# Kernel tuning notes

Measured on AMD Instinct MI355X. Metric: run time of the kernel, lower is better.

The kernel has to match this reference:

```python
import jax, jax.numpy as jnp
import numpy as np

B, T, G, P = 16, 256, 1024, 16          # batch, num_tf, num_genes, peaks per gene
N, GO_DIM = 4096, 6                      # num_gos, go_dim (hard-coded in module)
HEADS, OUT_CH = 2, 4                     # selfGATConv(go_dim, 4, heads=2)
E = 65536                                # num edges
NUM_OUT = 32


def lrelu(x, slope):
    return jnp.where(x >= 0, x, slope * x)


def setup_inputs() -> dict:
    ks = jax.random.split(jax.random.key(0), 12)
    x = jax.random.normal(ks[0], (B, T, G * P), dtype=jnp.float32)
    edge_index = jax.random.randint(ks[1], (2, E), 0, N, dtype=jnp.int64)
    # per-gene subNet: Linear(num_peak*num_tf, 1) -> weight [G, T, P], bias [G]
    W_sub = jax.random.normal(ks[2], (G, T, P), dtype=jnp.float32) * 0.02
    b_sub = jax.random.normal(ks[3], (G,), dtype=jnp.float32) * 0.02
    fc1_weight = jax.random.normal(ks[4], (N * GO_DIM, G), dtype=jnp.float32) * 0.02
    mask = (jax.random.uniform(ks[5], (N, G)) < 0.05).astype(jnp.float32)
    mask_rep = jnp.repeat(mask, GO_DIM, axis=0)  # [N*GO_DIM, G]
    fc1_bias = jax.random.normal(ks[6], (N * GO_DIM,), dtype=jnp.float32) * 0.02
    gat_weight = jax.random.normal(ks[7], (GO_DIM, HEADS * OUT_CH), dtype=jnp.float32) * 0.3
    gat_att = jax.random.normal(ks[8], (1, 1, HEADS, 2 * OUT_CH), dtype=jnp.float32) * 0.3
    gat_bias = jax.random.normal(ks[9], (OUT_CH,), dtype=jnp.float32) * 0.02
    out_weight = jax.random.normal(ks[10], (NUM_OUT, N * OUT_CH), dtype=jnp.float32) * 0.02
    out_bias = jax.random.normal(ks[11], (NUM_OUT,), dtype=jnp.float32) * 0.02
    return {"x": x, "edge_index": edge_index, "W_sub": W_sub, "b_sub": b_sub,
            "fc1_weight": fc1_weight, "mask_rep": mask_rep, "fc1_bias": fc1_bias,
            "gat_weight": gat_weight, "gat_att": gat_att, "gat_bias": gat_bias,
            "out_weight": out_weight, "out_bias": out_bias}


def reference(x, edge_index, W_sub, b_sub, fc1_weight, mask_rep, fc1_bias,
              gat_weight, gat_att, gat_bias, out_weight, out_bias):
    # --- per-gene subnets (uniform num_peaks -> block-diag as one einsum) ---
    xg = x.reshape(B, T, G, P)                        # contiguous cut blocks
    x_cat = jnp.einsum('btgp,gtp->bg', xg, W_sub) + b_sub   # [B, G]
    x_cat = lrelu(x_cat, 0.01)                        # nn.LeakyReLU default
    # --- masked dense linear -> GO-term hidden layer ---
    h = x_cat @ (fc1_weight * mask_rep).T + fc1_bias  # [B, N*GO_DIM]
    h = lrelu(h, 0.01)
    h = h.reshape(B, GO_DIM, N).transpose(2, 0, 1)    # [N, B, GO_DIM]
    # --- selfGATConv: gather -> leaky_relu score -> seg-softmax -> scatter-mean ---
    hn = (h @ gat_weight).reshape(N, B, HEADS, OUT_CH)  # [N, B, H, C]
    src, dst = edge_index[0], edge_index[1]
    x_j = hn[src]                                     # [E, B, H, C]
    x_i = hn[dst]
    att = gat_att[0, 0]                               # [H, 2C]
    alpha = (jnp.einsum('ebhc,hc->ebh', x_i, att[:, :OUT_CH]) +
             jnp.einsum('ebhc,hc->ebh', x_j, att[:, OUT_CH:]))
    alpha = lrelu(alpha, 0.2)                         # negative_slope=0.2
    amax = jax.ops.segment_max(alpha, dst, num_segments=N)
    alpha = jnp.exp(alpha - amax[dst])
    denom = jax.ops.segment_sum(alpha, dst, num_segments=N)
    alpha = alpha / denom[dst]                        # per-destination softmax
    msg = x_j * alpha[..., None]                      # [E, B, H, C]
    summed = jax.ops.segment_sum(msg, dst, num_segments=N)
    cnt = jax.ops.segment_sum(jnp.ones((E,), jnp.float32), dst, num_segments=N)
    aggr = summed / jnp.maximum(cnt, 1.0)[:, None, None, None]  # aggr='mean'
    aggr = aggr.mean(axis=2) + gat_bias               # concat=False: mean heads -> [N, B, C]
    # --- readout ---
    o = aggr.transpose(1, 2, 0).reshape(B, OUT_CH * N)
    o = lrelu(o, 0.01)                                # dropout is identity in eval
    return o @ out_weight.T + out_bias                # [B, NUM_OUT]
```

## Files before the change

### kernel.cpp

```cpp
#include <hip/hip_runtime.h>
#include <math.h>

#define KB 16
#define KT 256
#define KG 1024
#define KP 16
#define KN 4096
#define KGO 6
#define KH 2
#define KC 4
#define KE 65536
#define KOUT 32

__device__ __forceinline__ float lrelu(float x, float s) { return x >= 0.f ? x : s * x; }

__global__ __launch_bounds__(1024) void k1_subnet(const float* __restrict__ x,
                                                  const float* __restrict__ Wsub,
                                                  const float* __restrict__ bsub,
                                                  float* __restrict__ xcat,
                                                  int* __restrict__ cnt) {
    if (blockIdx.x >= 256) {
        int t = threadIdx.x;
#pragma unroll
        for (int i = 0; i < 4; ++i) cnt[t + i * 1024] = 0;
        return;
    }
    int wk  = ((blockIdx.x & 7) << 5) | (blockIdx.x >> 3);
    int tid = threadIdx.x;
    int sub = tid >> 8;
    int u   = tid & 255;
    int gc  = wk >> 4;
    int b   = wk & 15;
    int g0  = gc * 64;
    int g   = g0 + (u >> 2);
    int p4  = (u & 3) * 4;
    const float* xb = x + (size_t)b * (KT * KG * KP) + (size_t)g0 * KP + u * 4;
    const float* wg = Wsub + (size_t)g * (KT * KP) + p4;
    float4 acc = make_float4(0.f, 0.f, 0.f, 0.f);
    int t0 = sub * 64;
#pragma unroll 4
    for (int i = 0; i < 64; ++i) {
        int t = t0 + i;
        float4 xv = *(const float4*)(xb + (size_t)t * (KG * KP));
        float4 wv = *(const float4*)(wg + (size_t)t * KP);
        acc.x += xv.x * wv.x; acc.y += xv.y * wv.y;
        acc.z += xv.z * wv.z; acc.w += xv.w * wv.w;
    }
    float s = acc.x + acc.y + acc.z + acc.w;
    s += __shfl_xor(s, 1, 64);
    s += __shfl_xor(s, 2, 64);
    __shared__ float part[4][64];
    if ((u & 3) == 0) part[sub][u >> 2] = s;
    __syncthreads();
    if (tid < 64) {
        float v = part[0][tid] + part[1][tid] + part[2][tid] + part[3][tid];
        xcat[b * KG + g0 + tid] = lrelu(v + bsub[g0 + tid], 0.01f);
    }
}

__global__ __launch_bounds__(256) void k2_fc1(const float* __restrict__ w,
                                              const float* __restrict__ mask,
                                              const float* __restrict__ bias,
                                              const float* __restrict__ xcat,
                                              float* __restrict__ ht) {
    int wid = threadIdx.x >> 6;
    int lane = threadIdx.x & 63;
    int b0 = wid * 4;
    float4 xcr[4][4];
#pragma unroll
    for (int bb = 0; bb < 4; ++bb)
#pragma unroll
        for (int i = 0; i < 4; ++i)
            xcr[bb][i] = *(const float4*)(xcat + (b0 + bb) * KG + i * 256 + lane * 4);

    int mj_cur = -1;
    float4 mreg[4];
    for (int r = 0; r < 16; ++r) {
        int j = blockIdx.x * 16 + r;
        int mj = j / 6;
        if (mj != mj_cur) {
            const float* mr = mask + (size_t)(mj * 6) * KG;
#pragma unroll
            for (int i = 0; i < 4; ++i)
                mreg[i] = *(const float4*)(mr + i * 256 + lane * 4);
            mj_cur = mj;
        }
        const float* wr = w + (size_t)j * KG;
        float acc0 = 0.f, acc1 = 0.f, acc2 = 0.f, acc3 = 0.f;
#pragma unroll
        for (int i = 0; i < 4; ++i) {
            float4 wv = *(const float4*)(wr + i * 256 + lane * 4);
            float4 mv = mreg[i];
            float px = wv.x * mv.x, py = wv.y * mv.y, pz = wv.z * mv.z, pw = wv.w * mv.w;
            acc0 += px * xcr[0][i].x + py * xcr[0][i].y + pz * xcr[0][i].z + pw * xcr[0][i].w;
            acc1 += px * xcr[1][i].x + py * xcr[1][i].y + pz * xcr[1][i].z + pw * xcr[1][i].w;
            acc2 += px * xcr[2][i].x + py * xcr[2][i].y + pz * xcr[2][i].z + pw * xcr[2][i].w;
            acc3 += px * xcr[3][i].x + py * xcr[3][i].y + pz * xcr[3][i].z + pw * xcr[3][i].w;
        }
#pragma unroll
        for (int m = 1; m < 64; m <<= 1) {
            acc0 += __shfl_xor(acc0, m, 64);
            acc1 += __shfl_xor(acc1, m, 64);
            acc2 += __shfl_xor(acc2, m, 64);
            acc3 += __shfl_xor(acc3, m, 64);
        }
        if (lane == 0) {
            float bj = bias[j];
            int d = j >> 12;
            int n = j & 4095;
            float* hp = ht + ((size_t)n * KB) * KGO + d;
            hp[(b0 + 0) * KGO] = lrelu(acc0 + bj, 0.01f);
            hp[(b0 + 1) * KGO] = lrelu(acc1 + bj, 0.01f);
            hp[(b0 + 2) * KGO] = lrelu(acc2 + bj, 0.01f);
            hp[(b0 + 3) * KGO] = lrelu(acc3 + bj, 0.01f);
        }
    }
}

__global__ __launch_bounds__(256) void k3_gatw(const float* __restrict__ ht,
                                               const float* __restrict__ gw,
                                               const float* __restrict__ att,
                                               float* __restrict__ hn,
                                               float* __restrict__ si,
                                               float* __restrict__ sj) {
    __shared__ float cgw[48];
    __shared__ float catt[16];
    int t = threadIdx.x;
    if (t < 48) cgw[t] = gw[t];
    else if (t < 64) catt[t - 48] = att[t - 48];
    __syncthreads();
    int idx = blockIdx.x * 256 + t;
    float h6[6];
#pragma unroll
    for (int d = 0; d < 6; ++d) h6[d] = ht[(size_t)idx * KGO + d];
    float o[8];
#pragma unroll
    for (int hc = 0; hc < 8; ++hc) {
        float v = 0.f;
#pragma unroll
        for (int d = 0; d < 6; ++d) v += h6[d] * cgw[d * 8 + hc];
        o[hc] = v;
        hn[(size_t)idx * 8 + hc] = v;
    }
#pragma unroll
    for (int hh = 0; hh < 2; ++hh) {
        float vi = 0.f, vj = 0.f;
#pragma unroll
        for (int c = 0; c < 4; ++c) {
            vi += o[hh * 4 + c] * catt[hh * 8 + c];
            vj += o[hh * 4 + c] * catt[hh * 8 + 4 + c];
        }
        si[idx * 2 + hh] = vi;
        sj[idx * 2 + hh] = vj;
    }
}

__global__ __launch_bounds__(256) void k4a_hist(const int* __restrict__ e32,
                                                int* __restrict__ cnt) {
    __shared__ int smode;
    int t = threadIdx.x;
    int e = blockIdx.x * 256 + t;
    int hi = e32[2 * e + 1];
    if (t == 0) smode = 1;
    __syncthreads();
    if (hi != 0) smode = 0;
    __syncthreads();
    int mode = smode;
    int d = mode ? e32[2 * (KE + e)] : e32[KE + e];
    atomicAdd(&cnt[d], 1);
}

__global__ __launch_bounds__(1024) void k4b_scan(const int* __restrict__ cnt,
                                                 int* __restrict__ off,
                                                 int* __restrict__ cur) {
    __shared__ int buf[2][1024];
    int t = threadIdx.x;
    int c0 = cnt[t * 4 + 0], c1 = cnt[t * 4 + 1], c2 = cnt[t * 4 + 2], c3 = cnt[t * 4 + 3];
    int s = c0 + c1 + c2 + c3;
    buf[0][t] = s;
    __syncthreads();
    int pb = 0;
    for (int d = 1; d < 1024; d <<= 1) {
        int v = buf[pb][t];
        if (t >= d) v += buf[pb][t - d];
        buf[1 - pb][t] = v;
        pb = 1 - pb;
        __syncthreads();
    }
    int incl = buf[pb][t];
    int base = incl - s;
    int o0 = base, o1 = base + c0, o2 = base + c0 + c1, o3 = base + c0 + c1 + c2;
    off[t * 4 + 0] = o0; off[t * 4 + 1] = o1; off[t * 4 + 2] = o2; off[t * 4 + 3] = o3;
    cur[t * 4 + 0] = o0; cur[t * 4 + 1] = o1; cur[t * 4 + 2] = o2; cur[t * 4 + 3] = o3;
    if (t == 1023) off[KN] = incl;
}

__global__ __launch_bounds__(256) void k4c_scatter(const int* __restrict__ e32,
                                                   int* __restrict__ cur,
                                                   int* __restrict__ csr) {
    __shared__ int smode;
    int t = threadIdx.x;
    int e = blockIdx.x * 256 + t;
    int hi = e32[2 * e + 1];
    if (t == 0) smode = 1;
    __syncthreads();
    if (hi != 0) smode = 0;
    __syncthreads();
    int mode = smode;
    int d = mode ? e32[2 * (KE + e)] : e32[KE + e];
    int s = mode ? e32[2 * e] : e32[e];
    int p = atomicAdd(&cur[d], 1);
    csr[p] = s;
}

__global__ __launch_bounds__(256) void k5_gat(const int* __restrict__ offs,
                                              const int* __restrict__ csr,
                                              const float* __restrict__ si,
                                              const float* __restrict__ sj,
                                              const float* __restrict__ hn,
                                              const float* __restrict__ gbias,
                                              float* __restrict__ aggr) {
    int n = blockIdx.x;
    int t = threadIdx.x;
    int p = t >> 3;
    int s = t & 7;
    int b = p >> 1, h = p & 1;
    int off = offs[n];
    int deg = offs[n + 1] - off;
    __shared__ float red[32][4];
    float l = 0.f, a0 = 0.f, a1 = 0.f, a2 = 0.f, a3 = 0.f;
    if (deg > 0) {
        float sib = si[(n * KB + b) * 2 + h];
        float m = -1e30f;
        for (int i = s; i < deg; i += 8) {
            int sv = csr[off + i];
            float a = sib + sj[(sv * KB + b) * 2 + h];
            a = a >= 0.f ? a : 0.2f * a;
            m = fmaxf(m, a);
        }
        m = fmaxf(m, __shfl_xor(m, 1, 64));
        m = fmaxf(m, __shfl_xor(m, 2, 64));
        m = fmaxf(m, __shfl_xor(m, 4, 64));
        for (int i = s; i < deg; i += 8) {
            int sv = csr[off + i];
            float a = sib + sj[(sv * KB + b) * 2 + h];
            a = a >= 0.f ? a : 0.2f * a;
            float wgt = expf(a - m);
            l += wgt;
            float4 hv = *(const float4*)(hn + ((size_t)(sv * KB + b)) * 8 + h * 4);
            a0 += wgt * hv.x; a1 += wgt * hv.y; a2 += wgt * hv.z; a3 += wgt * hv.w;
        }
#pragma unroll
        for (int d = 1; d <= 4; d <<= 1) {
            l  += __shfl_xor(l,  d, 64);
            a0 += __shfl_xor(a0, d, 64);
            a1 += __shfl_xor(a1, d, 64);
            a2 += __shfl_xor(a2, d, 64);
            a3 += __shfl_xor(a3, d, 64);
        }
    }
    if (s == 0) {
        float inv = (deg > 0) ? 1.f / l : 0.f;
        red[p][0] = a0 * inv; red[p][1] = a1 * inv;
        red[p][2] = a2 * inv; red[p][3] = a3 * inv;
    }
    __syncthreads();
    if (t < 64) {
        int bb = t >> 2, c = t & 3;
        float v = gbias[c];
        if (deg > 0)
            v += 0.5f * (red[bb * 2 + 0][c] + red[bb * 2 + 1][c]) / (float)deg;
        aggr[bb * (KC * KN) + c * KN + n] = v;
    }
}

__global__ __launch_bounds__(256) void k6_out(const float* __restrict__ aggr,
                                              const float* __restrict__ ow,
                                              const float* __restrict__ obias,
                                              float* __restrict__ out) {
    int b = blockIdx.x >> 5;
    int k = blockIdx.x & 31;
    int t = threadIdx.x;
    const float* ar = aggr + (size_t)b * (KC * KN);
    const float* wr = ow + (size_t)k * (KC * KN);
    float sum = 0.f;
#pragma unroll 4
    for (int i = 0; i < 16; ++i) {
        int j = (i * 256 + t) * 4;
        float4 av = *(const float4*)(ar + j);
        float4 wv = *(const float4*)(wr + j);
        av.x = lrelu(av.x, 0.01f); av.y = lrelu(av.y, 0.01f);
        av.z = lrelu(av.z, 0.01f); av.w = lrelu(av.w, 0.01f);
        sum += av.x * wv.x + av.y * wv.y + av.z * wv.z + av.w * wv.w;
    }
#pragma unroll
    for (int d = 32; d > 0; d >>= 1) sum += __shfl_down(sum, d, 64);
    __shared__ float wsum[4];
    if ((t & 63) == 0) wsum[t >> 6] = sum;
    __syncthreads();
    if (t == 0) out[b * KOUT + k] = wsum[0] + wsum[1] + wsum[2] + wsum[3] + obias[k];
}

extern "C" void kernel_launch(void* const* d_in, const int* in_sizes, int n_in,
                              void* d_out, int out_size, void* d_ws, size_t ws_size,
                              hipStream_t stream) {
    const float* x     = (const float*)d_in[0];
    const int*   e32   = (const int*)d_in[1];
    const float* Wsub  = (const float*)d_in[2];
    const float* bsub  = (const float*)d_in[3];
    const float* fc1w  = (const float*)d_in[4];
    const float* maskr = (const float*)d_in[5];
    const float* fc1b  = (const float*)d_in[6];
    const float* gatw  = (const float*)d_in[7];
    const float* gata  = (const float*)d_in[8];
    const float* gatb  = (const float*)d_in[9];
    const float* outw  = (const float*)d_in[10];
    const float* outb  = (const float*)d_in[11];
    float* out = (float*)d_out;

    float* ws   = (float*)d_ws;
    float* xcat = ws;
    float* ht   = xcat + KB * KG;
    float* hn   = ht + (size_t)KN * KB * KGO;
    float* si   = hn + (size_t)KN * KB * KH * KC;
    float* sj   = si + (size_t)KN * KB * KH;
    float* aggr = sj + (size_t)KN * KB * KH;
    int* icnt  = (int*)(aggr + (size_t)KB * KC * KN);
    int* ioff  = icnt + KN;
    int* icur  = ioff + (KN + 16);
    int* icsr  = icur + KN;

    k1_subnet<<<257, 1024, 0, stream>>>(x, Wsub, bsub, xcat, icnt);
    k2_fc1<<<(KN * KGO) / 16, 256, 0, stream>>>(fc1w, maskr, fc1b, xcat, ht);
    k3_gatw<<<(KN * KB) / 256, 256, 0, stream>>>(ht, gatw, gata, hn, si, sj);
    k4a_hist<<<KE / 256, 256, 0, stream>>>(e32, icnt);
    k4b_scan<<<1, 1024, 0, stream>>>(icnt, ioff, icur);
    k4c_scatter<<<KE / 256, 256, 0, stream>>>(e32, icur, icsr);
    k5_gat<<<KN, 256, 0, stream>>>(ioff, icsr, si, sj, hn, gatb, aggr);
    k6_out<<<KB * KOUT, 256, 0, stream>>>(aggr, outw, outb, out);
}
```

Measured before the change: 538.3 us.

## Fuse GAT tail stages into one cooperative persistent kernel with grid syncs

Merges the GAT projection, edge histogram, scan, CSR scatter, attention aggregation and readout kernels into a single cooperative kernel. Stages are separated by grid-wide syncs, and the grid size comes from occupancy. The aim is to remove six kernel launch overheads and the gaps between them. In exchange it adds grid.sync costs, limits each stage to the persistent block count, and runs the scan on a single block with 256 threads instead of 1024.

```diff
diff --git a/kernel.cpp b/kernel.cpp
--- a/kernel.cpp
+++ b/kernel.cpp
@@ -1,5 +1,8 @@
 #include <hip/hip_runtime.h>
+#include <hip/hip_cooperative_groups.h>
 #include <math.h>
+
+namespace cg = cooperative_groups;
 
 #define KB 16
 #define KT 256
@@ -117,188 +120,202 @@
     }
 }
 
-__global__ __launch_bounds__(256) void k3_gatw(const float* __restrict__ ht,
-                                               const float* __restrict__ gw,
-                                               const float* __restrict__ att,
-                                               float* __restrict__ hn,
-                                               float* __restrict__ si,
-                                               float* __restrict__ sj) {
+__global__ __launch_bounds__(256) void k_tail(const float* __restrict__ ht,
+                                              const float* __restrict__ gw,
+                                              const float* __restrict__ att,
+                                              const int*   __restrict__ e32,
+                                              const float* __restrict__ gbias,
+                                              const float* __restrict__ ow,
+                                              const float* __restrict__ obias,
+                                              float* __restrict__ hn,
+                                              float* __restrict__ si,
+                                              float* __restrict__ sj,
+                                              int* __restrict__ cnt,
+                                              int* __restrict__ off,
+                                              int* __restrict__ cur,
+                                              int* __restrict__ csr,
+                                              float* __restrict__ aggr,
+                                              float* __restrict__ out) {
+    cg::grid_group grid = cg::this_grid();
+    const int tid  = threadIdx.x;
+    const int bid  = blockIdx.x;
+    const int nb   = gridDim.x;
+    const int gtid = bid * 256 + tid;
+    const int gsz  = nb * 256;
+
     __shared__ float cgw[48];
     __shared__ float catt[16];
-    int t = threadIdx.x;
-    if (t < 48) cgw[t] = gw[t];
-    else if (t < 64) catt[t - 48] = att[t - 48];
+    __shared__ int   smode;
+    __shared__ int   sbuf[2][256];
+    __shared__ float red[32][4];
+    __shared__ float wsum[4];
+
+    if (tid < 48) cgw[tid] = gw[tid];
+    else if (tid < 64) catt[tid - 48] = att[tid - 48];
     __syncthreads();
-    int idx = blockIdx.x * 256 + t;
-    float h6[6];
-#pragma unroll
-    for (int d = 0; d < 6; ++d) h6[d] = ht[(size_t)idx * KGO + d];
-    float o[8];
-#pragma unroll
-    for (int hc = 0; hc < 8; ++hc) {
-        float v = 0.f;
-#pragma unroll
-        for (int d = 0; d < 6; ++d) v += h6[d] * cgw[d * 8 + hc];
-        o[hc] = v;
-        hn[(size_t)idx * 8 + hc] = v;
-    }
-#pragma unroll
-    for (int hh = 0; hh < 2; ++hh) {
-        float vi = 0.f, vj = 0.f;
-#pragma unroll
-        for (int c = 0; c < 4; ++c) {
-            vi += o[hh * 4 + c] * catt[hh * 8 + c];
-            vj += o[hh * 4 + c] * catt[hh * 8 + 4 + c];
-        }
-        si[idx * 2 + hh] = vi;
-        sj[idx * 2 + hh] = vj;
-    }
-}
-
-__global__ __launch_bounds__(256) void k4a_hist(const int* __restrict__ e32,
-                                                int* __restrict__ cnt) {
-    __shared__ int smode;
-    int t = threadIdx.x;
-    int e = blockIdx.x * 256 + t;
-    int hi = e32[2 * e + 1];
-    if (t == 0) smode = 1;
-    __syncthreads();
-    if (hi != 0) smode = 0;
-    __syncthreads();
-    int mode = smode;
-    int d = mode ? e32[2 * (KE + e)] : e32[KE + e];
-    atomicAdd(&cnt[d], 1);
-}
-
-__global__ __launch_bounds__(1024) void k4b_scan(const int* __restrict__ cnt,
-                                                 int* __restrict__ off,
-                                                 int* __restrict__ cur) {
-    __shared__ int buf[2][1024];
-    int t = threadIdx.x;
-    int c0 = cnt[t * 4 + 0], c1 = cnt[t * 4 + 1], c2 = cnt[t * 4 + 2], c3 = cnt[t * 4 + 3];
-    int s = c0 + c1 + c2 + c3;
-    buf[0][t] = s;
-    __syncthreads();
-    int pb = 0;
-    for (int d = 1; d < 1024; d <<= 1) {
-        int v = buf[pb][t];
-        if (t >= d) v += buf[pb][t - d];
-        buf[1 - pb][t] = v;
-        pb = 1 - pb;
-        __syncthreads();
-    }
-    int incl = buf[pb][t];
-    int base = incl - s;
-    int o0 = base, o1 = base + c0, o2 = base + c0 + c1, o3 = base + c0 + c1 + c2;
-    off[t * 4 + 0] = o0; off[t * 4 + 1] = o1; off[t * 4 + 2] = o2; off[t * 4 + 3] = o3;
-    cur[t * 4 + 0] = o0; cur[t * 4 + 1] = o1; cur[t * 4 + 2] = o2; cur[t * 4 + 3] = o3;
-    if (t == 1023) off[KN] = incl;
-}
-
-__global__ __launch_bounds__(256) void k4c_scatter(const int* __restrict__ e32,
-                                                   int* __restrict__ cur,
-                                                   int* __restrict__ csr) {
-    __shared__ int smode;
-    int t = threadIdx.x;
-    int e = blockIdx.x * 256 + t;
-    int hi = e32[2 * e + 1];
-    if (t == 0) smode = 1;
-    __syncthreads();
-    if (hi != 0) smode = 0;
-    __syncthreads();
-    int mode = smode;
-    int d = mode ? e32[2 * (KE + e)] : e32[KE + e];
-    int s = mode ? e32[2 * e] : e32[e];
-    int p = atomicAdd(&cur[d], 1);
-    csr[p] = s;
-}
-
-__global__ __launch_bounds__(256) void k5_gat(const int* __restrict__ offs,
-                                              const int* __restrict__ csr,
-                                              const float* __restrict__ si,
-                                              const float* __restrict__ sj,
-                                              const float* __restrict__ hn,
-                                              const float* __restrict__ gbias,
-                                              float* __restrict__ aggr) {
-    int n = blockIdx.x;
-    int t = threadIdx.x;
-    int p = t >> 3;
-    int s = t & 7;
-    int b = p >> 1, h = p & 1;
-    int off = offs[n];
-    int deg = offs[n + 1] - off;
-    __shared__ float red[32][4];
-    float l = 0.f, a0 = 0.f, a1 = 0.f, a2 = 0.f, a3 = 0.f;
-    if (deg > 0) {
-        float sib = si[(n * KB + b) * 2 + h];
-        float m = -1e30f;
-        for (int i = s; i < deg; i += 8) {
-            int sv = csr[off + i];
-            float a = sib + sj[(sv * KB + b) * 2 + h];
-            a = a >= 0.f ? a : 0.2f * a;
-            m = fmaxf(m, a);
-        }
-        m = fmaxf(m, __shfl_xor(m, 1, 64));
-        m = fmaxf(m, __shfl_xor(m, 2, 64));
-        m = fmaxf(m, __shfl_xor(m, 4, 64));
-        for (int i = s; i < deg; i += 8) {
-            int sv = csr[off + i];
-            float a = sib + sj[(sv * KB + b) * 2 + h];
-            a = a >= 0.f ? a : 0.2f * a;
-            float wgt = expf(a - m);
-            l += wgt;
-            float4 hv = *(const float4*)(hn + ((size_t)(sv * KB + b)) * 8 + h * 4);
-            a0 += wgt * hv.x; a1 += wgt * hv.y; a2 += wgt * hv.z; a3 += wgt * hv.w;
-        }
-#pragma unroll
-        for (int d = 1; d <= 4; d <<= 1) {
-            l  += __shfl_xor(l,  d, 64);
-            a0 += __shfl_xor(a0, d, 64);
-            a1 += __shfl_xor(a1, d, 64);
-            a2 += __shfl_xor(a2, d, 64);
-            a3 += __shfl_xor(a3, d, 64);
-        }
-    }
-    if (s == 0) {
-        float inv = (deg > 0) ? 1.f / l : 0.f;
-        red[p][0] = a0 * inv; red[p][1] = a1 * inv;
-        red[p][2] = a2 * inv; red[p][3] = a3 * inv;
-    }
-    __syncthreads();
-    if (t < 64) {
-        int bb = t >> 2, c = t & 3;
-        float v = gbias[c];
-        if (deg > 0)
-            v += 0.5f * (red[bb * 2 + 0][c] + red[bb * 2 + 1][c]) / (float)deg;
-        aggr[bb * (KC * KN) + c * KN + n] = v;
-    }
-}
-
-__global__ __launch_bounds__(256) void k6_out(const float* __restrict__ aggr,
-                                              const float* __restrict__ ow,
-                                              const float* __restrict__ obias,
-                                              float* __restrict__ out) {
-    int b = blockIdx.x >> 5;
-    int k = blockIdx.x & 31;
-    int t = threadIdx.x;
-    const float* ar = aggr + (size_t)b * (KC * KN);
-    const float* wr = ow + (size_t)k * (KC * KN);
-    float sum = 0.f;
+    for (int idx = gtid; idx < KN * KB; idx += gsz) {
+        float h6[6];
+#pragma unroll
+        for (int d = 0; d < 6; ++d) h6[d] = ht[(size_t)idx * KGO + d];
+        float o[8];
+#pragma unroll
+        for (int hc = 0; hc < 8; ++hc) {
+            float v = 0.f;
+#pragma unroll
+            for (int d = 0; d < 6; ++d) v += h6[d] * cgw[d * 8 + hc];
+            o[hc] = v;
+            hn[(size_t)idx * 8 + hc] = v;
+        }
+#pragma unroll
+        for (int hh = 0; hh < 2; ++hh) {
+            float vi = 0.f, vj = 0.f;
+#pragma unroll
+            for (int c = 0; c < 4; ++c) {
+                vi += o[hh * 4 + c] * catt[hh * 8 + c];
+                vj += o[hh * 4 + c] * catt[hh * 8 + 4 + c];
+            }
+            si[idx * 2 + hh] = vi;
+            sj[idx * 2 + hh] = vj;
+        }
+    }
+
+    for (int base = bid * 256; base < KE; base += gsz) {
+        int e = base + tid;
+        int hi = e32[2 * e + 1];
+        if (tid == 0) smode = 1;
+        __syncthreads();
+        if (hi != 0) smode = 0;
+        __syncthreads();
+        int mode = smode;
+        int d = mode ? e32[2 * (KE + e)] : e32[KE + e];
+        atomicAdd(&cnt[d], 1);
+        __syncthreads();
+    }
+    __threadfence();
+    grid.sync();
+
+    if (bid == 0) {
+        int c[16];
+        int s = 0;
+#pragma unroll
+        for (int i = 0; i < 16; ++i) { c[i] = cnt[tid * 16 + i]; s += c[i]; }
+        sbuf[0][tid] = s;
+        __syncthreads();
+        int pb = 0;
+        for (int d = 1; d < 256; d <<= 1) {
+            int v = sbuf[pb][tid];
+            if (tid >= d) v += sbuf[pb][tid - d];
+            sbuf[1 - pb][tid] = v;
+            pb = 1 - pb;
+            __syncthreads();
+        }
+        int incl = sbuf[pb][tid];
+        int run = incl - s;
+#pragma unroll
+        for (int i = 0; i < 16; ++i) {
+            off[tid * 16 + i] = run;
+            cur[tid * 16 + i] = run;
+            run += c[i];
+        }
+        if (tid == 255) off[KN] = incl;
+    }
+    __threadfence();
+    grid.sync();
+
+    for (int base = bid * 256; base < KE; base += gsz) {
+        int e = base + tid;
+        int hi = e32[2 * e + 1];
+        if (tid == 0) smode = 1;
+        __syncthreads();
+        if (hi != 0) smode = 0;
+        __syncthreads();
+        int mode = smode;
+        int d = mode ? e32[2 * (KE + e)] : e32[KE + e];
+        int s = mode ? e32[2 * e] : e32[e];
+        int p = atomicAdd(&cur[d], 1);
+        csr[p] = s;
+        __syncthreads();
+    }
+    __threadfence();
+    grid.sync();
+
+    for (int n = bid; n < KN; n += nb) {
+        int p = tid >> 3;
+        int s = tid & 7;
+        int b = p >> 1, h = p & 1;
+        int o0 = off[n];
+        int deg = off[n + 1] - o0;
+        float l = 0.f, a0 = 0.f, a1 = 0.f, a2 = 0.f, a3 = 0.f;
+        if (deg > 0) {
+            float sib = si[(n * KB + b) * 2 + h];
+            float m = -1e30f;
+            for (int i = s; i < deg; i += 8) {
+                int sv = csr[o0 + i];
+                float a = sib + sj[(sv * KB + b) * 2 + h];
+                a = a >= 0.f ? a : 0.2f * a;
+                m = fmaxf(m, a);
+            }
+            m = fmaxf(m, __shfl_xor(m, 1, 64));
+            m = fmaxf(m, __shfl_xor(m, 2, 64));
+            m = fmaxf(m, __shfl_xor(m, 4, 64));
+            for (int i = s; i < deg; i += 8) {
+                int sv = csr[o0 + i];
+                float a = sib + sj[(sv * KB + b) * 2 + h];
+                a = a >= 0.f ? a : 0.2f * a;
+                float wgt = expf(a - m);
+                l += wgt;
+                float4 hv = *(const float4*)(hn + ((size_t)(sv * KB + b)) * 8 + h * 4);
+                a0 += wgt * hv.x; a1 += wgt * hv.y; a2 += wgt * hv.z; a3 += wgt * hv.w;
+            }
+#pragma unroll
+            for (int d = 1; d <= 4; d <<= 1) {
+                l  += __shfl_xor(l,  d, 64);
+                a0 += __shfl_xor(a0, d, 64);
+                a1 += __shfl_xor(a1, d, 64);
+                a2 += __shfl_xor(a2, d, 64);
+                a3 += __shfl_xor(a3, d, 64);
+            }
+        }
+        if (s == 0) {
+            float inv = (deg > 0) ? 1.f / l : 0.f;
+            red[p][0] = a0 * inv; red[p][1] = a1 * inv;
+            red[p][2] = a2 * inv; red[p][3] = a3 * inv;
+        }
+        __syncthreads();
+        if (tid < 64) {
+            int bb = tid >> 2, c = tid & 3;
+            float v = gbias[c];
+            if (deg > 0)
+                v += 0.5f * (red[bb * 2 + 0][c] + red[bb * 2 + 1][c]) / (float)deg;
+            aggr[bb * (KC * KN) + c * KN + n] = v;
+        }
+        __syncthreads();
+    }
+    __threadfence();
+    grid.sync();
+
+    for (int pair = bid; pair < KB * KOUT; pair += nb) {
+        int b = pair >> 5;
+        int k = pair & 31;
+        const float* ar = aggr + (size_t)b * (KC * KN);
+        const float* wr = ow + (size_t)k * (KC * KN);
+        float sum = 0.f;
 #pragma unroll 4
-    for (int i = 0; i < 16; ++i) {
-        int j = (i * 256 + t) * 4;
-        float4 av = *(const float4*)(ar + j);
-        float4 wv = *(const float4*)(wr + j);
-        av.x = lrelu(av.x, 0.01f); av.y = lrelu(av.y, 0.01f);
-        av.z = lrelu(av.z, 0.01f); av.w = lrelu(av.w, 0.01f);
-        sum += av.x * wv.x + av.y * wv.y + av.z * wv.z + av.w * wv.w;
-    }
-#pragma unroll
-    for (int d = 32; d > 0; d >>= 1) sum += __shfl_down(sum, d, 64);
-    __shared__ float wsum[4];
-    if ((t & 63) == 0) wsum[t >> 6] = sum;
-    __syncthreads();
-    if (t == 0) out[b * KOUT + k] = wsum[0] + wsum[1] + wsum[2] + wsum[3] + obias[k];
+        for (int i = 0; i < 16; ++i) {
+            int j = (i * 256 + tid) * 4;
+            float4 av = *(const float4*)(ar + j);
+            float4 wv = *(const float4*)(wr + j);
+            av.x = lrelu(av.x, 0.01f); av.y = lrelu(av.y, 0.01f);
+            av.z = lrelu(av.z, 0.01f); av.w = lrelu(av.w, 0.01f);
+            sum += av.x * wv.x + av.y * wv.y + av.z * wv.z + av.w * wv.w;
+        }
+#pragma unroll
+        for (int d = 32; d > 0; d >>= 1) sum += __shfl_down(sum, d, 64);
+        if ((tid & 63) == 0) wsum[tid >> 6] = sum;
+        __syncthreads();
+        if (tid == 0) out[b * KOUT + k] = wsum[0] + wsum[1] + wsum[2] + wsum[3] + obias[k];
+        __syncthreads();
+    }
 }
 
 extern "C" void kernel_launch(void* const* d_in, const int* in_sizes, int n_in,
@@ -330,12 +347,24 @@
     int* icur  = ioff + (KN + 16);
     int* icsr  = icur + KN;
 
+    static int g_nblk = 0;
+    if (g_nblk == 0) {
+        int occ = 0;
+        hipOccupancyMaxActiveBlocksPerMultiprocessor(&occ, k_tail, 256, 0);
+        if (occ < 1) occ = 1;
+        long nb = (long)occ * 256;
+        if (nb > 4096) nb = 4096;
+        g_nblk = (int)nb;
+    }
+
     k1_subnet<<<257, 1024, 0, stream>>>(x, Wsub, bsub, xcat, icnt);
     k2_fc1<<<(KN * KGO) / 16, 256, 0, stream>>>(fc1w, maskr, fc1b, xcat, ht);
-    k3_gatw<<<(KN * KB) / 256, 256, 0, stream>>>(ht, gatw, gata, hn, si, sj);
-    k4a_hist<<<KE / 256, 256, 0, stream>>>(e32, icnt);
-    k4b_scan<<<1, 1024, 0, stream>>>(icnt, ioff, icur);
-    k4c_scatter<<<KE / 256, 256, 0, stream>>>(e32, icur, icsr);
-    k5_gat<<<KN, 256, 0, stream>>>(ioff, icsr, si, sj, hn, gatb, aggr);
-    k6_out<<<KB * KOUT, 256, 0, stream>>>(aggr, outw, outb, out);
+
+    void* args[] = {(void*)&ht, (void*)&gatw, (void*)&gata, (void*)&e32,
+                    (void*)&gatb, (void*)&outw, (void*)&outb,
+                    (void*)&hn, (void*)&si, (void*)&sj,
+                    (void*)&icnt, (void*)&ioff, (void*)&icur, (void*)&icsr,
+                    (void*)&aggr, (void*)&out};
+    hipLaunchCooperativeKernel((const void*)k_tail, dim3(g_nblk), dim3(256),
+                               args, 0, stream);
 }
```

Result: slower. 949.2 us (+76.3%).
